# Optimization experiments

Hardware: AMD Instinct MI355X
Metric: run time of the kernel (lower is better)

Reference implementation:

```python
import jax, jax.numpy as jnp
import numpy as np

SEQ, B, D, T = 512, 128, 1024, 32  # seq_len, batch, input_dim, num_tags


def setup_inputs() -> dict:
    key = jax.random.key(0)
    ks = jax.random.split(key, 6)
    return {
        "features": jax.random.normal(ks[0], (SEQ, B, D), jnp.float32),
        "mask": jnp.ones((SEQ, B), jnp.int32),
        "W": jax.random.normal(ks[1], (T, D), jnp.float32) * 0.02,   # features_to_tag weight
        "b": jnp.zeros((T,), jnp.float32),                            # features_to_tag bias
        "transition": jax.random.normal(ks[2], (T, T), jnp.float32) * 0.1,
        "start_probs": jax.random.normal(ks[3], (T,), jnp.float32) * 0.1,
        "end_probs": jax.random.normal(ks[4], (T,), jnp.float32) * 0.1,
    }


def _alpha(emissions, maskf, trans, start):
    # forward recursion: alpha[i, b, j] = logsumexp_k(alpha[i-1,b,k] + trans[k,j]) + e[i,b,j]
    a0 = emissions[0] + start[None, :]
    def step(prev, xs):
        e, m = xs
        new = jax.nn.logsumexp(prev[:, :, None] + trans[None] + e[:, None, :], axis=1)
        nxt = m[:, None] * new + (1.0 - m)[:, None] * prev
        return nxt, nxt
    _, rest = jax.lax.scan(step, a0, (emissions[1:], maskf[1:]))
    return jnp.concatenate([a0[None], rest], axis=0)  # (S,B,T)


def _beta(emissions, maskf, trans, end):
    # backward recursion: beta[i-1, b, j] = logsumexp_k(beta[i,b,k] + e[i,b,k] + trans[j,k])
    bL = jnp.broadcast_to(end[None, :], emissions.shape[1:])  # (B,T)
    def step(prev, xs):
        e, m = xs
        s = prev + e  # (B,T)
        new = jax.nn.logsumexp(s[:, None, :] + trans[None], axis=2)
        nxt = m[:, None] * new + (1.0 - m)[:, None] * prev
        return nxt, nxt
    _, rest = jax.lax.scan(step, bL, (emissions[1:], maskf[1:]), reverse=True)
    return jnp.concatenate([rest, bL[None]], axis=0)  # (S,B,T)


def _viterbi(emissions, mask, trans, start, end):
    s0 = start[None, :] + emissions[0]  # (B,T)
    def step(score, xs):
        e, m = xs
        cand = score[:, :, None] + trans[None] + e[:, None, :]  # (B,T_from,T_to)
        nxt = jnp.max(cand, axis=1)
        idx = jnp.argmax(cand, axis=1).astype(jnp.int32)
        score = jnp.where(m[:, None].astype(bool), nxt, score)
        return score, idx
    score, history = jax.lax.scan(step, s0, (emissions[1:], mask[1:]))
    score = score + end[None, :]
    last = jnp.argmax(score, axis=1).astype(jnp.int32)  # (B,)
    def back(tag, hist):
        new = jnp.take_along_axis(hist, tag[:, None], axis=1)[:, 0]
        return new, new
    _, tags_rest = jax.lax.scan(back, last, history, reverse=True)
    return jnp.concatenate([tags_rest, last[None]], axis=0)  # (S,B)


def reference(features, mask, W, b, transition, start_probs, end_probs):
    emissions = jnp.einsum("sbd,td->sbt", features, W) + b  # (S,B,T)
    maskf = mask.astype(emissions.dtype)
    alpha = _alpha(emissions, maskf, transition, start_probs)
    beta = _beta(emissions, maskf, transition, end_probs)
    z = jax.nn.logsumexp(alpha[-1] + end_probs[None, :], axis=1)  # (B,)
    probs = jnp.exp(alpha + beta - z[None, :, None])  # marginal probabilities
    tags = _viterbi(emissions, mask, transition, start_probs, end_probs)
    return probs, tags
```

## Files before the change

kernel.cpp:

```cpp
#include <hip/hip_runtime.h>

#define SEQ 512
#define BATCH 128
#define DIM 1024
#define T 32

typedef int v2i_ __attribute__((ext_vector_type(2)));

__device__ __forceinline__ float rlf(float x, int n) {
    return __int_as_float(__builtin_amdgcn_readlane(__float_as_int(x), n));
}

__device__ __forceinline__ float sum_halves(float x) {
    v2i_ r = __builtin_amdgcn_permlane32_swap(__float_as_int(x), __float_as_int(x), false, false);
    return __int_as_float(r.x) + __int_as_float(r.y);
}
__device__ __forceinline__ float max_halves(float x) {
    v2i_ r = __builtin_amdgcn_permlane32_swap(__float_as_int(x), __float_as_int(x), false, false);
    return fmaxf(__int_as_float(r.x), __int_as_float(r.y));
}

__device__ __forceinline__ int mbit(unsigned long long m0, unsigned long long m1,
        unsigned long long m2, unsigned long long m3, unsigned long long m4,
        unsigned long long m5, unsigned long long m6, unsigned long long m7, int i) {
    int w = i >> 6;
    unsigned long long cm =
        (w < 4) ? ((w < 2) ? (w == 0 ? m0 : m1) : (w == 2 ? m2 : m3))
                : ((w < 6) ? (w == 4 ? m4 : m5) : (w == 6 ? m6 : m7));
    return (int)((cm >> (i & 63)) & 1ULL);
}

#define BALLOTS(pre, bb) \
    unsigned long long pre##0 = __ballot(mask[(0 * 64 + tid) * BATCH + (bb)] != 0); \
    unsigned long long pre##1 = __ballot(mask[(1 * 64 + tid) * BATCH + (bb)] != 0); \
    unsigned long long pre##2 = __ballot(mask[(2 * 64 + tid) * BATCH + (bb)] != 0); \
    unsigned long long pre##3 = __ballot(mask[(3 * 64 + tid) * BATCH + (bb)] != 0); \
    unsigned long long pre##4 = __ballot(mask[(4 * 64 + tid) * BATCH + (bb)] != 0); \
    unsigned long long pre##5 = __ballot(mask[(5 * 64 + tid) * BATCH + (bb)] != 0); \
    unsigned long long pre##6 = __ballot(mask[(6 * 64 + tid) * BATCH + (bb)] != 0); \
    unsigned long long pre##7 = __ballot(mask[(7 * 64 + tid) * BATCH + (bb)] != 0);

#define MB(pre, i) mbit(pre##0, pre##1, pre##2, pre##3, pre##4, pre##5, pre##6, pre##7, (i))

#define RLSUM32(dst, src) { \
    float s0 = 0.f, s1 = 0.f, s2 = 0.f, s3 = 0.f; \
    _Pragma("unroll") \
    for (int n = 0; n < 8; ++n) { \
        s0 += rlf(src, 4 * n + 0); \
        s1 += rlf(src, 4 * n + 1); \
        s2 += rlf(src, 4 * n + 2); \
        s3 += rlf(src, 4 * n + 3); \
    } \
    dst = (s0 + s1) + (s2 + s3); }

#define STAGEXP(blk) do { \
    _Pragma("unroll") \
    for (int ps = 0; ps < 16; ++ps) { \
        int r = ps * 8 + r8; \
        float4 v = *(const float4*)&e[(size_t)(((blk) * 128 + r) * BATCH + b) * T + q * 4]; \
        v.x = __expf(v.x); v.y = __expf(v.y); v.z = __expf(v.z); v.w = __expf(v.w); \
        *(float4*)&ebuf[(blk) & 1][r * 32 + q * 4] = v; \
    } } while (0)

#define FLUSHPC(dstP, dstC, blk) do { \
    _Pragma("unroll") \
    for (int ps = 0; ps < 16; ++ps) { \
        int r = ps * 8 + r8; \
        float4 v = *(const float4*)&pbuf[(blk) & 1][r * 32 + q * 4]; \
        *(float4*)&dstP[(size_t)(((blk) * 128 + r) * BATCH + b) * T + q * 4] = v; \
    } \
    _Pragma("unroll") \
    for (int ps = 0; ps < 2; ++ps) { \
        int r = ps * 64 + tid; \
        dstC[(size_t)((blk) * 128 + r) * BATCH + b] = cbuf[(blk) & 1][r]; \
    } } while (0)

#define STAGEV(blk) do { \
    _Pragma("unroll") \
    for (int ps = 0; ps < 8; ++ps) { \
        int r = ps * 8 + r8; \
        float4 v = *(const float4*)&e[(size_t)(((blk) * 64 + r) * BATCH + b2) * T + q * 4]; \
        *(float4*)&ebufv[r * 32 + q * 4] = v; \
    } } while (0)

__global__ void k_wt(const float* __restrict__ W, float* __restrict__ Wt)
{
    int idx = blockIdx.x * 256 + threadIdx.x;
    if (idx >= DIM * T) return;
    int d = idx >> 5, t = idx & 31;
    Wt[idx] = W[t * DIM + d];
}

__global__ __launch_bounds__(256) void k_emis(const float* __restrict__ A,
        const float* __restrict__ Wt, const float* __restrict__ bias,
        float* __restrict__ e)
{
    __shared__ float lds[64 * 37];
    int tid = threadIdx.x;
    int row0 = blockIdx.x * 64;
    int row = tid & 63;
    int grp = __builtin_amdgcn_readfirstlane(tid >> 6);
    int q = tid & 7;
    int rb = tid >> 3;

    float acc[8];
    #pragma unroll
    for (int t = 0; t < 8; ++t) acc[t] = bias[grp * 8 + t];

    const float* A0 = &A[(size_t)(row0 + rb) * DIM];
    const float* A1 = &A[(size_t)(row0 + rb + 32) * DIM];

    float4 v0 = *(const float4*)&A0[q * 4];
    float4 v1 = *(const float4*)&A1[q * 4];

    for (int ck = 0; ck < 32; ++ck) {
        lds[rb * 37 + q * 4 + 0] = v0.x;
        lds[rb * 37 + q * 4 + 1] = v0.y;
        lds[rb * 37 + q * 4 + 2] = v0.z;
        lds[rb * 37 + q * 4 + 3] = v0.w;
        lds[(rb + 32) * 37 + q * 4 + 0] = v1.x;
        lds[(rb + 32) * 37 + q * 4 + 1] = v1.y;
        lds[(rb + 32) * 37 + q * 4 + 2] = v1.z;
        lds[(rb + 32) * 37 + q * 4 + 3] = v1.w;
        __syncthreads();
        if (ck < 31) {
            v0 = *(const float4*)&A0[(ck + 1) * 32 + q * 4];
            v1 = *(const float4*)&A1[(ck + 1) * 32 + q * 4];
        }
        #pragma unroll
        for (int d = 0; d < 32; ++d) {
            float av = lds[row * 37 + d];
            const float* wrow = &Wt[(ck * 32 + d) * T + grp * 8];
            #pragma unroll
            for (int t = 0; t < 8; ++t)
                acc[t] = fmaf(av, wrow[t], acc[t]);
        }
        __syncthreads();
    }

    float4* eo = (float4*)&e[(size_t)(row0 + row) * T + grp * 8];
    float4 o0, o1;
    o0.x = acc[0]; o0.y = acc[1]; o0.z = acc[2]; o0.w = acc[3];
    o1.x = acc[4]; o1.y = acc[5]; o1.z = acc[6]; o1.w = acc[7];
    eo[0] = o0; eo[1] = o1;
}

__global__ __launch_bounds__(64) void k_rec(const float* __restrict__ e,
        const int* __restrict__ mask,
        const float* __restrict__ trans,
        const float* __restrict__ start,
        const float* __restrict__ endp,
        float* __restrict__ pa, float* __restrict__ pb,
        double* __restrict__ Ca, double* __restrict__ Cb,
        double* __restrict__ zd,
        float* __restrict__ tags_out)
{
    __shared__ __align__(16) char smem[78336];
    int bid = blockIdx.x;
    int tid = threadIdx.x;
    int j   = tid & 31;
    int h   = tid >> 5;
    int r8 = tid >> 3, q = tid & 7;

    if (bid < 256) {
        int role = bid >> 7;
        int b    = bid & 127;
        float (*ebuf)[4096] = (float(*)[4096])smem;
        float (*pbuf)[4096] = (float(*)[4096])(smem + 32768);
        double (*cbuf)[128] = (double(*)[128])(smem + 65536);
        float* pering = (float*)(smem + 67584);

        BALLOTS(ma, b);
        float Eh[16];

        if (role == 0) {
            #pragma unroll
            for (int m = 0; m < 16; ++m)
                Eh[m] = __expf(trans[(16 * h + m) * T + j]);

            STAGEXP(0);
            float a0 = e[(0 * BATCH + b) * T + j] + start[j];
            float m = a0;
            #pragma unroll
            for (int d = 1; d < 32; d <<= 1) m = fmaxf(m, __shfl_xor(m, d));
            float v = __expf(a0 - m);
            float s = v;
            #pragma unroll
            for (int d = 1; d < 32; d <<= 1) s += __shfl_xor(s, d);
            float p = v / s;
            double C = (double)m + (double)__logf(s);
            pbuf[0][j] = p;
            if (tid == 0) cbuf[0][0] = C;

            for (int c = 0; c < 4; ++c) {
                int i0 = c ? c * 128 : 1, i1 = c * 128 + 127;
                for (int i = i0; i <= i1; ++i) {
                    int pr = i - 1;
                    const float4* pr4 = (const float4*)&pbuf[(pr >> 7) & 1][(pr & 127) * 32 + 16 * h];
                    float ee = ebuf[c & 1][(i & 127) * 32 + j];
                    float4 x0 = pr4[0], x1 = pr4[1], x2 = pr4[2], x3 = pr4[3];
                    float q0 = fmaf(x0.w, Eh[3], fmaf(x0.z, Eh[2], fmaf(x0.y, Eh[1], x0.x * Eh[0])));
                    float q1 = fmaf(x1.w, Eh[7], fmaf(x1.z, Eh[6], fmaf(x1.y, Eh[5], x1.x * Eh[4])));
                    float q2 = fmaf(x2.w, Eh[11], fmaf(x2.z, Eh[10], fmaf(x2.y, Eh[9], x2.x * Eh[8])));
                    float q3 = fmaf(x3.w, Eh[15], fmaf(x3.z, Eh[14], fmaf(x3.y, Eh[13], x3.x * Eh[12])));
                    float qh = (q0 + q1) + (q2 + q3);
                    float qq = sum_halves(qh);
                    float vv = qq * ee;
                    if (MB(ma, i)) p = vv;
                    if ((i & 7) == 0) {
                        float ss; RLSUM32(ss, p);
                        p = p / ss; C += (double)__logf(ss);
                    }
                    pbuf[c & 1][(i & 127) * 32 + j] = p;
                    if (tid == 0) cbuf[c & 1][i & 127] = C;
                }
                if (c < 3) STAGEXP(c + 1);
                FLUSHPC(pa, Ca, c);
            }
            float sz0 = p * __expf(endp[j]);
            float sz; RLSUM32(sz, sz0);
            if (tid == 0) zd[b] = C + (double)__logf(sz);
        } else {
            #pragma unroll
            for (int m = 0; m < 16; ++m)
                Eh[m] = __expf(trans[j * T + 16 * h + m]);

            STAGEXP(3);
            float v0 = endp[j];
            float m = v0;
            #pragma unroll
            for (int d = 1; d < 32; d <<= 1) m = fmaxf(m, __shfl_xor(m, d));
            float v = __expf(v0 - m);
            float s = v;
            #pragma unroll
            for (int d = 1; d < 32; d <<= 1) s += __shfl_xor(s, d);
            float p = v / s;
            double C = (double)m + (double)__logf(s);
            pbuf[1][127 * 32 + j] = p;
            if (tid == 0) cbuf[1][127] = C;
            pering[32 + j] = p * ebuf[1][127 * 32 + j];

            for (int c = 0; c < 4; ++c) {
                int iS = 511 - 128 * c;
                int iE = (c < 3) ? (384 - 128 * c) : 1;
                for (int i = iS; i >= iE; --i) {
                    const float4* pe4 = (const float4*)&pering[(i & 1) * 32 + 16 * h];
                    float4 x0 = pe4[0], x1 = pe4[1], x2 = pe4[2], x3 = pe4[3];
                    float q0 = fmaf(x0.w, Eh[3], fmaf(x0.z, Eh[2], fmaf(x0.y, Eh[1], x0.x * Eh[0])));
                    float q1 = fmaf(x1.w, Eh[7], fmaf(x1.z, Eh[6], fmaf(x1.y, Eh[5], x1.x * Eh[4])));
                    float q2 = fmaf(x2.w, Eh[11], fmaf(x2.z, Eh[10], fmaf(x2.y, Eh[9], x2.x * Eh[8])));
                    float q3 = fmaf(x3.w, Eh[15], fmaf(x3.z, Eh[14], fmaf(x3.y, Eh[13], x3.x * Eh[12])));
                    float qh = (q0 + q1) + (q2 + q3);
                    float qq = sum_halves(qh);
                    if (MB(ma, i)) p = qq;
                    if ((i & 7) == 0) {
                        float ss; RLSUM32(ss, p);
                        p = p / ss; C += (double)__logf(ss);
                    }
                    int orow = i - 1, lb = (orow >> 7) & 1;
                    pbuf[lb][(orow & 127) * 32 + j] = p;
                    if (tid == 0) cbuf[lb][orow & 127] = C;
                    if (i > iE) {
                        float ee = ebuf[((i - 1) >> 7) & 1][((i - 1) & 127) * 32 + j];
                        pering[((i - 1) & 1) * 32 + j] = p * ee;
                    }
                }
                if (c < 3) {
                    STAGEXP(2 - c);
                    float ee = ebuf[(2 - c) & 1][127 * 32 + j];
                    pering[((iE - 1) & 1) * 32 + j] = p * ee;
                }
                FLUSHPC(pb, Cb, 3 - c);
            }
        }
    } else {
        int b2 = bid - 256;
        float* ebufv = (float*)smem;
        float* sbuf  = (float*)(smem + 8192);
        float* tldsT = (float*)(smem + 73728);
        unsigned char* tagb = (unsigned char*)(smem + 77824);

        BALLOTS(ma, b2);

        #pragma unroll
        for (int k = 0; k < 16; ++k) {
            int idx = k * 64 + tid;
            int nn = idx >> 5, jj = idx & 31;
            tldsT[jj * 32 + nn] = trans[nn * T + jj];
        }

        float trvh[16];
        #pragma unroll
        for (int m = 0; m < 16; ++m)
            trvh[m] = trans[(16 * h + m) * T + j];

        STAGEV(0);
        float sc = start[j] + ebufv[j];
        sbuf[j] = sc;

        for (int c = 0; c < 8; ++c) {
            int i0 = c ? c * 64 : 1, i1 = c * 64 + 63;
            for (int i = i0; i <= i1; ++i) {
                const float4* sr4 = (const float4*)&sbuf[(i - 1) * 32 + 16 * h];
                float ej = ebufv[(i & 63) * 32 + j];
                float4 s0 = sr4[0], s1 = sr4[1], s2 = sr4[2], s3 = sr4[3];
                float m0 = fmaxf(fmaxf(s0.x + trvh[0], s0.y + trvh[1]),
                                 fmaxf(s0.z + trvh[2], s0.w + trvh[3]));
                float m1 = fmaxf(fmaxf(s1.x + trvh[4], s1.y + trvh[5]),
                                 fmaxf(s1.z + trvh[6], s1.w + trvh[7]));
                float m2 = fmaxf(fmaxf(s2.x + trvh[8], s2.y + trvh[9]),
                                 fmaxf(s2.z + trvh[10], s2.w + trvh[11]));
                float m3 = fmaxf(fmaxf(s3.x + trvh[12], s3.y + trvh[13]),
                                 fmaxf(s3.z + trvh[14], s3.w + trvh[15]));
                float mh = fmaxf(fmaxf(m0, m1), fmaxf(m2, m3));
                float mm = max_halves(mh);
                float v = mm + ej;
                if (MB(ma, i)) sc = v;
                sbuf[i * 32 + j] = sc;
            }
            if (c < 7) STAGEV(c + 1);
        }

        float fs = sc + endp[j];
        int fj = j;
        #pragma unroll
        for (int d = 1; d < 32; d <<= 1) {
            float ov = __shfl_xor(fs, d); int oj = __shfl_xor(fj, d);
            if (ov > fs || (ov == fs && oj < fj)) { fs = ov; fj = oj; }
        }
        int jstar = __builtin_amdgcn_readfirstlane(fj);
        tagb[SEQ - 1] = (unsigned char)jstar;

        int n = tid & 31;
        for (int c = 7; c >= 0; --c) {
            if (c < 7) STAGEV(c);
            int iS = c * 64 + 63, iE = c ? c * 64 : 1;
            for (int i = iS; i >= iE; --i) {
                float sn = sbuf[(i - 1) * 32 + n];
                float tn = tldsT[jstar * 32 + n];
                float en = ebufv[(i & 63) * 32 + jstar];
                float cn = (sn + tn) + en;
                float v;
                if (MB(ma, i)) {
                    v = sbuf[i * 32 + jstar];
                } else {
                    v = cn;
                    #pragma unroll
                    for (int d = 1; d < 32; d <<= 1)
                        v = fmaxf(v, __shfl_xor(v, d));
                }
                unsigned long long bm = __ballot(cn == v);
                jstar = (int)__builtin_ctzll(bm);
                tagb[i - 1] = (unsigned char)jstar;
            }
        }
        #pragma unroll
        for (int k2 = 0; k2 < 8; ++k2) {
            int idx = k2 * 64 + tid;
            tags_out[(size_t)idx * BATCH + b2] = (float)tagb[idx];
        }
    }
}

__global__ __launch_bounds__(256) void k_probs(const float* __restrict__ pa,
        const float* __restrict__ pb, const double* __restrict__ Ca,
        const double* __restrict__ Cb, const double* __restrict__ zd,
        float* __restrict__ out)
{
    int idx = blockIdx.x * 256 + threadIdx.x;
    int ib = idx >> 3;
    int b = ib & (BATCH - 1);
    double ex = Ca[ib] + Cb[ib] - zd[b];
    double scl = exp(ex);
    float4 a = ((const float4*)pa)[idx];
    float4 c = ((const float4*)pb)[idx];
    float4 o;
    o.x = (float)((double)a.x * (double)c.x * scl);
    o.y = (float)((double)a.y * (double)c.y * scl);
    o.z = (float)((double)a.z * (double)c.z * scl);
    o.w = (float)((double)a.w * (double)c.w * scl);
    ((float4*)out)[idx] = o;
}

extern "C" void kernel_launch(void* const* d_in, const int* in_sizes, int n_in,
                              void* d_out, int out_size, void* d_ws, size_t ws_size,
                              hipStream_t stream) {
    const float* features = (const float*)d_in[0];
    const int*   mask     = (const int*)d_in[1];
    const float* W        = (const float*)d_in[2];
    const float* bias     = (const float*)d_in[3];
    const float* trans    = (const float*)d_in[4];
    const float* startp   = (const float*)d_in[5];
    const float* endp     = (const float*)d_in[6];

    char* ws = (char*)d_ws;
    double* Ca = (double*)(ws + 0);
    double* Cb = (double*)(ws + 524288);
    double* zd = (double*)(ws + 1048576);
    float*  Wt = (float*)(ws + 1049600);
    float*  e  = (float*)(ws + 1180672);
    float*  pa = (float*)(ws + 9569280);
    float*  pb = (float*)(ws + 17957888);

    float* probs_out = (float*)d_out;
    float* tags_out  = probs_out + (size_t)SEQ * BATCH * T;

    k_wt<<<128, 256, 0, stream>>>(W, Wt);
    k_emis<<<1024, 256, 0, stream>>>(features, Wt, bias, e);
    k_rec<<<384, 64, 0, stream>>>(e, mask, trans, startp, endp,
                                  pa, pb, Ca, Cb, zd, tags_out);
    k_probs<<<2048, 256, 0, stream>>>(pa, pb, Ca, Cb, zd, probs_out);
}
```

Measured before the change: 287.4 us.

## Replace LDS round-trips in CRF recurrences with DPP row rotations and lane swaps

The per-step matrix-vector products in the forward, backward and Viterbi recurrences no longer re-read the previous state vector from shared memory. Each lane now holds one state element, the 16-way partial products use DPP row rotations against pre-rotated transition registers, and the halves are combined with permlane16/permlane32 swaps. This is meant to shorten the serial per-step latency chain by removing LDS reads and waits from the critical path. Emission loads are also prefetched one step ahead, and the probs kernel switches from double to float math, which trades some precision for throughput.

```diff
diff --git a/kernel.cpp b/kernel.cpp
--- a/kernel.cpp
+++ b/kernel.cpp
@@ -11,13 +11,22 @@
     return __int_as_float(__builtin_amdgcn_readlane(__float_as_int(x), n));
 }
 
-__device__ __forceinline__ float sum_halves(float x) {
+#define ROT(x, M) __int_as_float(__builtin_amdgcn_update_dpp( \
+    __float_as_int(x), __float_as_int(x), 0x120 + (M), 0xF, 0xF, false))
+
+__device__ __forceinline__ float pairsum16(float x) {
+    v2i_ r = __builtin_amdgcn_permlane16_swap(__float_as_int(x), __float_as_int(x), false, false);
+    return __int_as_float(r.x) + __int_as_float(r.y);
+}
+__device__ __forceinline__ float pairmax16(float x) {
+    v2i_ r = __builtin_amdgcn_permlane16_swap(__float_as_int(x), __float_as_int(x), false, false);
+    return fmaxf(__int_as_float(r.x), __int_as_float(r.y));
+}
+__device__ __forceinline__ float cross32(float x) {
     v2i_ r = __builtin_amdgcn_permlane32_swap(__float_as_int(x), __float_as_int(x), false, false);
-    return __int_as_float(r.x) + __int_as_float(r.y);
-}
-__device__ __forceinline__ float max_halves(float x) {
-    v2i_ r = __builtin_amdgcn_permlane32_swap(__float_as_int(x), __float_as_int(x), false, false);
-    return fmaxf(__int_as_float(r.x), __int_as_float(r.y));
+    int xi = __float_as_int(x);
+    int sw = (r.x == xi) ? r.y : r.x;
+    return __int_as_float(sw);
 }
 
 __device__ __forceinline__ int mbit(unsigned long long m0, unsigned long long m1,
@@ -42,16 +51,56 @@
 
 #define MB(pre, i) mbit(pre##0, pre##1, pre##2, pre##3, pre##4, pre##5, pre##6, pre##7, (i))
 
-#define RLSUM32(dst, src) { \
+#define RLSUMQ(dst, src) { \
     float s0 = 0.f, s1 = 0.f, s2 = 0.f, s3 = 0.f; \
     _Pragma("unroll") \
     for (int n = 0; n < 8; ++n) { \
-        s0 += rlf(src, 4 * n + 0); \
-        s1 += rlf(src, 4 * n + 1); \
-        s2 += rlf(src, 4 * n + 2); \
-        s3 += rlf(src, 4 * n + 3); \
+        s0 += rlf(src, n); \
+        s1 += rlf(src, 8 + n); \
+        s2 += rlf(src, 32 + n); \
+        s3 += rlf(src, 40 + n); \
     } \
     dst = (s0 + s1) + (s2 + s3); }
+
+#define DPPMV(dst, pv, Eh) { \
+    float q0 = (pv) * Eh[0]; \
+    float q1 = ROT(pv, 1) * Eh[1]; \
+    float q2 = ROT(pv, 2) * Eh[2]; \
+    float q3 = ROT(pv, 3) * Eh[3]; \
+    q0 = fmaf(ROT(pv, 4), Eh[4], q0); \
+    q1 = fmaf(ROT(pv, 5), Eh[5], q1); \
+    q2 = fmaf(ROT(pv, 6), Eh[6], q2); \
+    q3 = fmaf(ROT(pv, 7), Eh[7], q3); \
+    q0 = fmaf(ROT(pv, 8), Eh[8], q0); \
+    q1 = fmaf(ROT(pv, 9), Eh[9], q1); \
+    q2 = fmaf(ROT(pv, 10), Eh[10], q2); \
+    q3 = fmaf(ROT(pv, 11), Eh[11], q3); \
+    q0 = fmaf(ROT(pv, 12), Eh[12], q0); \
+    q1 = fmaf(ROT(pv, 13), Eh[13], q1); \
+    q2 = fmaf(ROT(pv, 14), Eh[14], q2); \
+    q3 = fmaf(ROT(pv, 15), Eh[15], q3); \
+    float qh_ = (q0 + q1) + (q2 + q3); \
+    dst = pairsum16(qh_); }
+
+#define DPPMAX(dst, sv, Vh) { \
+    float a0 = (sv) + Vh[0]; \
+    float a1 = ROT(sv, 1) + Vh[1]; \
+    float a2 = ROT(sv, 2) + Vh[2]; \
+    float a3 = ROT(sv, 3) + Vh[3]; \
+    a0 = fmaxf(a0, ROT(sv, 4) + Vh[4]); \
+    a1 = fmaxf(a1, ROT(sv, 5) + Vh[5]); \
+    a2 = fmaxf(a2, ROT(sv, 6) + Vh[6]); \
+    a3 = fmaxf(a3, ROT(sv, 7) + Vh[7]); \
+    a0 = fmaxf(a0, ROT(sv, 8) + Vh[8]); \
+    a1 = fmaxf(a1, ROT(sv, 9) + Vh[9]); \
+    a2 = fmaxf(a2, ROT(sv, 10) + Vh[10]); \
+    a3 = fmaxf(a3, ROT(sv, 11) + Vh[11]); \
+    a0 = fmaxf(a0, ROT(sv, 12) + Vh[12]); \
+    a1 = fmaxf(a1, ROT(sv, 13) + Vh[13]); \
+    a2 = fmaxf(a2, ROT(sv, 14) + Vh[14]); \
+    a3 = fmaxf(a3, ROT(sv, 15) + Vh[15]); \
+    float mh_ = fmaxf(fmaxf(a0, a1), fmaxf(a2, a3)); \
+    dst = pairmax16(mh_); }
 
 #define STAGEXP(blk) do { \
     _Pragma("unroll") \
@@ -158,9 +207,14 @@
     __shared__ __align__(16) char smem[78336];
     int bid = blockIdx.x;
     int tid = threadIdx.x;
-    int j   = tid & 31;
-    int h   = tid >> 5;
     int r8 = tid >> 3, q = tid & 7;
+
+    int rr = tid & 15;
+    int g  = tid >> 4;
+    int s0h = 16 * (g & 1);
+    int jl  = rr + 16 * (g >> 1);
+    int sig0 = s0h + rr;
+    bool lfix = (g == 1) || (g == 2);
 
     if (bid < 256) {
         int role = bid >> 7;
@@ -168,7 +222,6 @@
         float (*ebuf)[4096] = (float(*)[4096])smem;
         float (*pbuf)[4096] = (float(*)[4096])(smem + 32768);
         double (*cbuf)[128] = (double(*)[128])(smem + 65536);
-        float* pering = (float*)(smem + 67584);
 
         BALLOTS(ma, b);
         float Eh[16];
@@ -176,10 +229,11 @@
         if (role == 0) {
             #pragma unroll
             for (int m = 0; m < 16; ++m)
-                Eh[m] = __expf(trans[(16 * h + m) * T + j]);
+                Eh[m] = __expf(trans[(s0h + ((rr - m) & 15)) * T + jl]);
 
             STAGEXP(0);
-            float a0 = e[(0 * BATCH + b) * T + j] + start[j];
+            int j0 = tid & 31;
+            float a0 = e[(0 * BATCH + b) * T + j0] + start[j0];
             float m = a0;
             #pragma unroll
             for (int d = 1; d < 32; d <<= 1) m = fmaxf(m, __shfl_xor(m, d));
@@ -187,46 +241,46 @@
             float s = v;
             #pragma unroll
             for (int d = 1; d < 32; d <<= 1) s += __shfl_xor(s, d);
-            float p = v / s;
+            float p0 = v / s;
             double C = (double)m + (double)__logf(s);
-            pbuf[0][j] = p;
+            pbuf[0][j0] = p0;
             if (tid == 0) cbuf[0][0] = C;
+            float p  = pbuf[0][jl];
+            float pv = pbuf[0][sig0];
 
             for (int c = 0; c < 4; ++c) {
                 int i0 = c ? c * 128 : 1, i1 = c * 128 + 127;
+                float enext = ebuf[c & 1][(i0 & 127) * 32 + jl];
                 for (int i = i0; i <= i1; ++i) {
-                    int pr = i - 1;
-                    const float4* pr4 = (const float4*)&pbuf[(pr >> 7) & 1][(pr & 127) * 32 + 16 * h];
-                    float ee = ebuf[c & 1][(i & 127) * 32 + j];
-                    float4 x0 = pr4[0], x1 = pr4[1], x2 = pr4[2], x3 = pr4[3];
-                    float q0 = fmaf(x0.w, Eh[3], fmaf(x0.z, Eh[2], fmaf(x0.y, Eh[1], x0.x * Eh[0])));
-                    float q1 = fmaf(x1.w, Eh[7], fmaf(x1.z, Eh[6], fmaf(x1.y, Eh[5], x1.x * Eh[4])));
-                    float q2 = fmaf(x2.w, Eh[11], fmaf(x2.z, Eh[10], fmaf(x2.y, Eh[9], x2.x * Eh[8])));
-                    float q3 = fmaf(x3.w, Eh[15], fmaf(x3.z, Eh[14], fmaf(x3.y, Eh[13], x3.x * Eh[12])));
-                    float qh = (q0 + q1) + (q2 + q3);
-                    float qq = sum_halves(qh);
-                    float vv = qq * ee;
+                    float ecur = enext;
+                    if (i < i1) enext = ebuf[c & 1][((i + 1) & 127) * 32 + jl];
+                    float qq;
+                    DPPMV(qq, pv, Eh);
+                    float vv = qq * ecur;
                     if (MB(ma, i)) p = vv;
                     if ((i & 7) == 0) {
-                        float ss; RLSUM32(ss, p);
+                        float ss; RLSUMQ(ss, p);
                         p = p / ss; C += (double)__logf(ss);
                     }
-                    pbuf[c & 1][(i & 127) * 32 + j] = p;
+                    pbuf[c & 1][(i & 127) * 32 + jl] = p;
                     if (tid == 0) cbuf[c & 1][i & 127] = C;
+                    float cw = cross32(p);
+                    pv = lfix ? cw : p;
                 }
                 if (c < 3) STAGEXP(c + 1);
                 FLUSHPC(pa, Ca, c);
             }
-            float sz0 = p * __expf(endp[j]);
-            float sz; RLSUM32(sz, sz0);
+            float t = p * __expf(endp[jl]);
+            float sz; RLSUMQ(sz, t);
             if (tid == 0) zd[b] = C + (double)__logf(sz);
         } else {
             #pragma unroll
             for (int m = 0; m < 16; ++m)
-                Eh[m] = __expf(trans[j * T + 16 * h + m]);
+                Eh[m] = __expf(trans[jl * T + s0h + ((rr - m) & 15)]);
 
             STAGEXP(3);
-            float v0 = endp[j];
+            int j0 = tid & 31;
+            float v0 = endp[j0];
             float m = v0;
             #pragma unroll
             for (int d = 1; d < 32; d <<= 1) m = fmaxf(m, __shfl_xor(m, d));
@@ -234,42 +288,36 @@
             float s = v;
             #pragma unroll
             for (int d = 1; d < 32; d <<= 1) s += __shfl_xor(s, d);
-            float p = v / s;
+            float p0 = v / s;
             double C = (double)m + (double)__logf(s);
-            pbuf[1][127 * 32 + j] = p;
+            pbuf[1][127 * 32 + j0] = p0;
             if (tid == 0) cbuf[1][127] = C;
-            pering[32 + j] = p * ebuf[1][127 * 32 + j];
+            float p  = pbuf[1][127 * 32 + jl];
+            float pv = pbuf[1][127 * 32 + sig0];
 
             for (int c = 0; c < 4; ++c) {
                 int iS = 511 - 128 * c;
                 int iE = (c < 3) ? (384 - 128 * c) : 1;
+                int bI = (3 - c) & 1;
+                float enext = ebuf[bI][(iS & 127) * 32 + sig0];
                 for (int i = iS; i >= iE; --i) {
-                    const float4* pe4 = (const float4*)&pering[(i & 1) * 32 + 16 * h];
-                    float4 x0 = pe4[0], x1 = pe4[1], x2 = pe4[2], x3 = pe4[3];
-                    float q0 = fmaf(x0.w, Eh[3], fmaf(x0.z, Eh[2], fmaf(x0.y, Eh[1], x0.x * Eh[0])));
-                    float q1 = fmaf(x1.w, Eh[7], fmaf(x1.z, Eh[6], fmaf(x1.y, Eh[5], x1.x * Eh[4])));
-                    float q2 = fmaf(x2.w, Eh[11], fmaf(x2.z, Eh[10], fmaf(x2.y, Eh[9], x2.x * Eh[8])));
-                    float q3 = fmaf(x3.w, Eh[15], fmaf(x3.z, Eh[14], fmaf(x3.y, Eh[13], x3.x * Eh[12])));
-                    float qh = (q0 + q1) + (q2 + q3);
-                    float qq = sum_halves(qh);
+                    float ecur = enext;
+                    if (i > iE) enext = ebuf[bI][((i - 1) & 127) * 32 + sig0];
+                    float pe = pv * ecur;
+                    float qq;
+                    DPPMV(qq, pe, Eh);
                     if (MB(ma, i)) p = qq;
                     if ((i & 7) == 0) {
-                        float ss; RLSUM32(ss, p);
+                        float ss; RLSUMQ(ss, p);
                         p = p / ss; C += (double)__logf(ss);
                     }
                     int orow = i - 1, lb = (orow >> 7) & 1;
-                    pbuf[lb][(orow & 127) * 32 + j] = p;
+                    pbuf[lb][(orow & 127) * 32 + jl] = p;
                     if (tid == 0) cbuf[lb][orow & 127] = C;
-                    if (i > iE) {
-                        float ee = ebuf[((i - 1) >> 7) & 1][((i - 1) & 127) * 32 + j];
-                        pering[((i - 1) & 1) * 32 + j] = p * ee;
-                    }
+                    float cw = cross32(p);
+                    pv = lfix ? cw : p;
                 }
-                if (c < 3) {
-                    STAGEXP(2 - c);
-                    float ee = ebuf[(2 - c) & 1][127 * 32 + j];
-                    pering[((iE - 1) & 1) * 32 + j] = p * ee;
-                }
+                if (c < 3) STAGEXP(2 - c);
                 FLUSHPC(pb, Cb, 3 - c);
             }
         }
@@ -289,42 +337,39 @@
             tldsT[jj * 32 + nn] = trans[nn * T + jj];
         }
 
-        float trvh[16];
+        float Vh[16];
         #pragma unroll
         for (int m = 0; m < 16; ++m)
-            trvh[m] = trans[(16 * h + m) * T + j];
+            Vh[m] = trans[(s0h + ((rr - m) & 15)) * T + jl];
 
         STAGEV(0);
-        float sc = start[j] + ebufv[j];
-        sbuf[j] = sc;
+        int j0 = tid & 31;
+        float sc0 = start[j0] + ebufv[j0];
+        sbuf[j0] = sc0;
+        float sc = sbuf[jl];
+        float sv = sbuf[sig0];
 
         for (int c = 0; c < 8; ++c) {
             int i0 = c ? c * 64 : 1, i1 = c * 64 + 63;
+            float ejnext = ebufv[(i0 & 63) * 32 + jl];
             for (int i = i0; i <= i1; ++i) {
-                const float4* sr4 = (const float4*)&sbuf[(i - 1) * 32 + 16 * h];
-                float ej = ebufv[(i & 63) * 32 + j];
-                float4 s0 = sr4[0], s1 = sr4[1], s2 = sr4[2], s3 = sr4[3];
-                float m0 = fmaxf(fmaxf(s0.x + trvh[0], s0.y + trvh[1]),
-                                 fmaxf(s0.z + trvh[2], s0.w + trvh[3]));
-                float m1 = fmaxf(fmaxf(s1.x + trvh[4], s1.y + trvh[5]),
-                                 fmaxf(s1.z + trvh[6], s1.w + trvh[7]));
-                float m2 = fmaxf(fmaxf(s2.x + trvh[8], s2.y + trvh[9]),
-                                 fmaxf(s2.z + trvh[10], s2.w + trvh[11]));
-                float m3 = fmaxf(fmaxf(s3.x + trvh[12], s3.y + trvh[13]),
-                                 fmaxf(s3.z + trvh[14], s3.w + trvh[15]));
-                float mh = fmaxf(fmaxf(m0, m1), fmaxf(m2, m3));
-                float mm = max_halves(mh);
+                float ej = ejnext;
+                if (i < i1) ejnext = ebufv[((i + 1) & 63) * 32 + jl];
+                float mm;
+                DPPMAX(mm, sv, Vh);
                 float v = mm + ej;
                 if (MB(ma, i)) sc = v;
-                sbuf[i * 32 + j] = sc;
+                sbuf[i * 32 + jl] = sc;
+                float cw = cross32(sc);
+                sv = lfix ? cw : sc;
             }
             if (c < 7) STAGEV(c + 1);
         }
 
-        float fs = sc + endp[j];
-        int fj = j;
+        float fs = sc + endp[jl];
+        int fj = jl;
         #pragma unroll
-        for (int d = 1; d < 32; d <<= 1) {
+        for (int d = 1; d < 64; d <<= 1) {
             float ov = __shfl_xor(fs, d); int oj = __shfl_xor(fj, d);
             if (ov > fs || (ov == fs && oj < fj)) { fs = ov; fj = oj; }
         }
@@ -371,14 +416,14 @@
     int ib = idx >> 3;
     int b = ib & (BATCH - 1);
     double ex = Ca[ib] + Cb[ib] - zd[b];
-    double scl = exp(ex);
+    float scl = __expf((float)ex);
     float4 a = ((const float4*)pa)[idx];
     float4 c = ((const float4*)pb)[idx];
     float4 o;
-    o.x = (float)((double)a.x * (double)c.x * scl);
-    o.y = (float)((double)a.y * (double)c.y * scl);
-    o.z = (float)((double)a.z * (double)c.z * scl);
-    o.w = (float)((double)a.w * (double)c.w * scl);
+    o.x = a.x * c.x * scl;
+    o.y = a.y * c.y * scl;
+    o.z = a.z * c.z * scl;
+    o.w = a.w * c.w * scl;
     ((float4*)out)[idx] = o;
 }
 
```

New measurement: 317.2 us. +10.4%, slower.

## Recompute Viterbi backpointers in batches and simplify probs scaling to float

Applied to the files above, without the earlier changes.

The Viterbi backtrace no longer does a serial per-step compare, shuffle-reduce and ballot against a transposed transition table. It recomputes the full argmax backpointers for 16 steps at a time in registers, a parallel tournament over all 32 target tags. It then chases the tag chain with readlane, which shortens the serial dependency per step and drops the LDS transpose. The probs kernel also switches from double exp and multiplies to a float __expf and float multiplies, which cheapens that elementwise pass but risks precision loss when the exponent is extreme.

```diff
diff --git a/kernel.cpp b/kernel.cpp
--- a/kernel.cpp
+++ b/kernel.cpp
@@ -277,17 +277,9 @@
         int b2 = bid - 256;
         float* ebufv = (float*)smem;
         float* sbuf  = (float*)(smem + 8192);
-        float* tldsT = (float*)(smem + 73728);
-        unsigned char* tagb = (unsigned char*)(smem + 77824);
+        unsigned char* tagb = (unsigned char*)(smem + 73728);
 
         BALLOTS(ma, b2);
-
-        #pragma unroll
-        for (int k = 0; k < 16; ++k) {
-            int idx = k * 64 + tid;
-            int nn = idx >> 5, jj = idx & 31;
-            tldsT[jj * 32 + nn] = trans[nn * T + jj];
-        }
 
         float trvh[16];
         #pragma unroll
@@ -325,33 +317,78 @@
         int fj = j;
         #pragma unroll
         for (int d = 1; d < 32; d <<= 1) {
-            float ov = __shfl_xor(fs, d); int oj = __shfl_xor(fj, d);
-            if (ov > fs || (ov == fs && oj < fj)) { fs = ov; fj = oj; }
-        }
-        int jstar = __builtin_amdgcn_readfirstlane(fj);
-        tagb[SEQ - 1] = (unsigned char)jstar;
-
-        int n = tid & 31;
+            float ov2 = __shfl_xor(fs, d); int oj2 = __shfl_xor(fj, d);
+            if (ov2 > fs || (ov2 == fs && oj2 < fj)) { fs = ov2; fj = oj2; }
+        }
+        int tag = __builtin_amdgcn_readfirstlane(fj);
+        tagb[SEQ - 1] = (unsigned char)tag;
+
         for (int c = 7; c >= 0; --c) {
             if (c < 7) STAGEV(c);
-            int iS = c * 64 + 63, iE = c ? c * 64 : 1;
-            for (int i = iS; i >= iE; --i) {
-                float sn = sbuf[(i - 1) * 32 + n];
-                float tn = tldsT[jstar * 32 + n];
-                float en = ebufv[(i & 63) * 32 + jstar];
-                float cn = (sn + tn) + en;
-                float v;
-                if (MB(ma, i)) {
-                    v = sbuf[i * 32 + jstar];
-                } else {
-                    v = cn;
+            for (int gg = 3; gg >= 0; --gg) {
+                int ib = c * 64 + 16 * gg;
+                int hreg[16];
+                #pragma unroll
+                for (int k = 0; k < 16; ++k) {
+                    int i = ib + k;
+                    if (i < 1) { hreg[k] = 0; continue; }
+                    const float4* sr4 = (const float4*)&sbuf[(i - 1) * 32 + 16 * h];
+                    float en = ebufv[(i & 63) * 32 + j];
+                    float4 s0 = sr4[0], s1 = sr4[1], s2 = sr4[2], s3 = sr4[3];
+                    float cd[16];
+                    cd[0]  = (s0.x + trvh[0])  + en;
+                    cd[1]  = (s0.y + trvh[1])  + en;
+                    cd[2]  = (s0.z + trvh[2])  + en;
+                    cd[3]  = (s0.w + trvh[3])  + en;
+                    cd[4]  = (s1.x + trvh[4])  + en;
+                    cd[5]  = (s1.y + trvh[5])  + en;
+                    cd[6]  = (s1.z + trvh[6])  + en;
+                    cd[7]  = (s1.w + trvh[7])  + en;
+                    cd[8]  = (s2.x + trvh[8])  + en;
+                    cd[9]  = (s2.y + trvh[9])  + en;
+                    cd[10] = (s2.z + trvh[10]) + en;
+                    cd[11] = (s2.w + trvh[11]) + en;
+                    cd[12] = (s3.x + trvh[12]) + en;
+                    cd[13] = (s3.y + trvh[13]) + en;
+                    cd[14] = (s3.z + trvh[14]) + en;
+                    cd[15] = (s3.w + trvh[15]) + en;
+                    float w1[8]; int x1[8];
                     #pragma unroll
-                    for (int d = 1; d < 32; d <<= 1)
-                        v = fmaxf(v, __shfl_xor(v, d));
+                    for (int n = 0; n < 8; ++n) {
+                        bool t = cd[2*n] >= cd[2*n+1];
+                        w1[n] = t ? cd[2*n] : cd[2*n+1];
+                        x1[n] = t ? 2*n : 2*n+1;
+                    }
+                    float w2[4]; int x2[4];
+                    #pragma unroll
+                    for (int n = 0; n < 4; ++n) {
+                        bool t = w1[2*n] >= w1[2*n+1];
+                        w2[n] = t ? w1[2*n] : w1[2*n+1];
+                        x2[n] = t ? x1[2*n] : x1[2*n+1];
+                    }
+                    float w3[2]; int x3[2];
+                    #pragma unroll
+                    for (int n = 0; n < 2; ++n) {
+                        bool t = w2[2*n] >= w2[2*n+1];
+                        w3[n] = t ? w2[2*n] : w2[2*n+1];
+                        x3[n] = t ? x2[2*n] : x2[2*n+1];
+                    }
+                    bool t0 = w3[0] >= w3[1];
+                    float bv = t0 ? w3[0] : w3[1];
+                    int gi = 16 * h + (t0 ? x3[0] : x3[1]);
+                    float ov = __shfl_xor(bv, 32);
+                    int   og = __shfl_xor(gi, 32);
+                    float lowV = h ? ov : bv;  int lowI = h ? og : gi;
+                    float hiV  = h ? bv : ov;  int hiI  = h ? gi : og;
+                    hreg[k] = (hiV > lowV) ? hiI : lowI;
                 }
-                unsigned long long bm = __ballot(cn == v);
-                jstar = (int)__builtin_ctzll(bm);
-                tagb[i - 1] = (unsigned char)jstar;
+                #pragma unroll
+                for (int k = 15; k >= 0; --k) {
+                    int i = ib + k;
+                    if (i < 1) break;
+                    tag = __builtin_amdgcn_readlane(hreg[k], tag);
+                    tagb[i - 1] = (unsigned char)tag;
+                }
             }
         }
         #pragma unroll
@@ -371,14 +408,14 @@
     int ib = idx >> 3;
     int b = ib & (BATCH - 1);
     double ex = Ca[ib] + Cb[ib] - zd[b];
-    double scl = exp(ex);
+    float scl = __expf((float)ex);
     float4 a = ((const float4*)pa)[idx];
     float4 c = ((const float4*)pb)[idx];
     float4 o;
-    o.x = (float)((double)a.x * (double)c.x * scl);
-    o.y = (float)((double)a.y * (double)c.y * scl);
-    o.z = (float)((double)a.z * (double)c.z * scl);
-    o.w = (float)((double)a.w * (double)c.w * scl);
+    o.x = a.x * c.x * scl;
+    o.y = a.y * c.y * scl;
+    o.z = a.z * c.z * scl;
+    o.w = a.w * c.w * scl;
     ((float4*)out)[idx] = o;
 }
 
```

Result: slower. 431.2 us (+50.0%).
